# Optimization experiments

Measured on AMD Instinct MI355X. Metric: run time of the kernel, lower is better.

## Reference

```python
import jax, jax.numpy as jnp
import numpy as np

OBS_LEN, BATCH, IN_DIM, HID = 20, 2048, 512, 1024


def setup_inputs() -> dict:
    key = jax.random.key(0)
    ks = jax.random.split(key, 9)
    s_ih = 1.0 / np.sqrt(HID)  # torch LSTMCell init scale (uniform); use normal*scale for simplicity
    return {
        "obs_traj": jax.random.normal(ks[0], (OBS_LEN, BATCH, 2), jnp.float32),
        "h0": jax.random.normal(ks[1], (BATCH, HID), jnp.float32),
        "c0": jax.random.normal(ks[2], (BATCH, HID), jnp.float32),
        "W_emb": jax.random.normal(ks[3], (IN_DIM, 2), jnp.float32) * 0.5,
        "b_emb": jax.random.normal(ks[4], (IN_DIM,), jnp.float32) * 0.5,
        "W_ih": jax.random.normal(ks[5], (4 * HID, IN_DIM), jnp.float32) * s_ih,
        "W_hh": jax.random.normal(ks[6], (4 * HID, HID), jnp.float32) * s_ih,
        "b_ih": jax.random.normal(ks[7], (4 * HID,), jnp.float32) * s_ih,
        "b_hh": jax.random.normal(ks[8], (4 * HID,), jnp.float32) * s_ih,
    }


def reference(obs_traj, h0, c0, W_emb, b_emb, W_ih, W_hh, b_ih, b_hh):
    # input embedding: Linear(2 -> IN_DIM) applied to all timesteps at once
    # [T, B, 2] @ [2, IN_DIM] -> [T, B, IN_DIM]
    x_emb = jnp.einsum('tbi,hi->tbh', obs_traj, W_emb) + b_emb
    x_emb = x_emb[:OBS_LEN]

    H = h0.shape[-1]
    bias = b_ih + b_hh  # fold both biases once

    def step(carry, x_t):
        h, c = carry
        # gates: [B, 4H], PyTorch gate order i, f, g, o
        gates = x_t @ W_ih.T + h @ W_hh.T + bias
        i_g = jax.nn.sigmoid(gates[:, 0 * H:1 * H])
        f_g = jax.nn.sigmoid(gates[:, 1 * H:2 * H])
        g_g = jnp.tanh(gates[:, 2 * H:3 * H])
        o_g = jax.nn.sigmoid(gates[:, 3 * H:4 * H])
        c_new = f_g * c + i_g * g_g
        h_new = o_g * jnp.tanh(c_new)
        return (h_new, c_new), None

    (h_final, _), _ = jax.lax.scan(step, (h0, c0), x_emb)
    return h_final
```

## Files before the change

### kernel.cpp

```cpp
#include <hip/hip_runtime.h>

#define B_SZ 2048
#define HID  1024
#define G4   4096
#define IN_D 512
#define T_LEN 20

#define POFF(r, q) ((r)*32 + ((((q) ^ (((r) >> 1) & 3))) << 3))

typedef __attribute__((ext_vector_type(8))) _Float16 f16x8;
typedef __attribute__((ext_vector_type(4))) float f32x4;
typedef const __attribute__((address_space(1))) void* gas_p;
typedef __attribute__((address_space(3))) void* las_p;

__device__ __forceinline__ float bf2f(ushort u){
  union { unsigned int i; float f; } v; v.i = ((unsigned int)u) << 16; return v.f;
}
__device__ __forceinline__ ushort f2bf(float f){
  union { float f; unsigned int i; } v; v.f = f;
  unsigned int r = v.i + 0x7fffu + ((v.i >> 16) & 1u);
  return (ushort)(r >> 16);
}
__device__ __forceinline__ ushort f2h(float f){
  _Float16 h = (_Float16)f;
  union { _Float16 h; ushort u; } v; v.h = h; return v.u;
}
__device__ __forceinline__ float rdv(const void* p, long idx, int fl){
  return fl ? ((const float*)p)[idx] : bf2f(((const ushort*)p)[idx]);
}
__device__ __forceinline__ float sigm(float x){ return 1.0f/(1.0f + __expf(-x)); }
__device__ __forceinline__ float tanh_f(float x){
  float e = __expf(2.0f*x);
  return 1.0f - 2.0f/(e + 1.0f);
}

__global__ void detect_dtype(const ushort* __restrict__ h0bits, int* __restrict__ flag){
  int weird = 0;
  for (int i = 0; i < 256; i += 2){
    float a = fabsf(bf2f(h0bits[i]));
    if (!(a >= 1e-8f && a <= 1e4f)) weird++;
  }
  *flag = (weird >= 32) ? 1 : 0;
}

__global__ void canon(const void* __restrict__ h0, const void* __restrict__ c0,
                      const void* __restrict__ whh, const int* __restrict__ flag,
                      ushort* __restrict__ hA,
                      float* __restrict__ c_state,
                      ushort* __restrict__ wpk){
  const int fl = *flag;
  long i = (long)blockIdx.x * 256 + threadIdx.x;
  const long N1 = (long)B_SZ * HID;
  const long N3 = (long)G4 * HID;
  if (i < N1){
    const int b = (int)(i >> 10), j = (int)(i & 1023);
    const int r = b & 127, q = (j >> 3) & 3;
    const long po = ((long)(b >> 7)*32 + (j >> 5))*4096 + POFF(r, q) + (j & 7);
    hA[po] = f2h(rdv(h0, i, fl));
    return;
  }
  i -= N1;
  if (i < N1){ c_state[i] = rdv(c0, i, fl); return; }
  i -= N1;
  if (i < N3){
    const int n = (int)(i >> 10), k = (int)(i & 1023);
    const int g = n >> 10, j = n & 1023;
    const int nb = j >> 5, r = g*32 + (j & 31);
    const int kt = k >> 5, q = (k >> 3) & 3;
    const long base = ((long)(nb*32 + kt))*4096 + POFF(r, q) + (k & 7);
    wpk[base] = f2h(rdv(whh, i, fl));
  }
}

__global__ void fold_emb(const void* __restrict__ Wih, const void* __restrict__ Wemb,
                         const void* __restrict__ bemb, const void* __restrict__ bih,
                         const void* __restrict__ bhh, const int* __restrict__ flag,
                         float* __restrict__ M0, float* __restrict__ M1, float* __restrict__ Beff){
  const int n = blockIdx.x;
  const int lane = threadIdx.x;
  const int fl = *flag;
  float s0 = 0.f, s1 = 0.f, sb = 0.f;
  for (int j = lane; j < IN_D; j += 64){
    float w  = rdv(Wih, (long)n*IN_D + j, fl);
    float e0 = rdv(Wemb, 2L*j, fl);
    float e1 = rdv(Wemb, 2L*j + 1, fl);
    float be = rdv(bemb, j, fl);
    s0 += w*e0; s1 += w*e1; sb += w*be;
  }
  #pragma unroll
  for (int off = 32; off > 0; off >>= 1){
    s0 += __shfl_down(s0, off, 64);
    s1 += __shfl_down(s1, off, 64);
    sb += __shfl_down(sb, off, 64);
  }
  if (lane == 0){
    M0[n] = s0; M1[n] = s1;
    Beff[n] = sb + rdv(bih, n, fl) + rdv(bhh, n, fl);
  }
}

__global__ __launch_bounds__(256, 4)
void lstm_step(const ushort* __restrict__ hin, ushort* __restrict__ hout,
               void* __restrict__ out_final,
               float* __restrict__ c_state,
               const ushort* __restrict__ wpk,
               const float* __restrict__ M0, const float* __restrict__ M1,
               const float* __restrict__ Beff,
               const void* __restrict__ obs_raw, int t_step,
               const int* __restrict__ flag, int is_final)
{
  __shared__ __align__(16) ushort lds[2*8192];

  const int tid  = threadIdx.x;
  const int wave = tid >> 6;
  const int lane = tid & 63;
  const int l15  = lane & 15;
  const int quad = lane >> 4;
  const int wm   = wave & 1;
  const int wn   = wave >> 1;

  const int bid = blockIdx.x;
  const int xcd = bid & 7, u = bid >> 3;
  const int mb  = ((xcd & 1) << 3) | (u & 7);
  const int nb  = ((xcd >> 1) << 3) | (u >> 3);
  const int n0  = nb << 5;

  f32x4 acc[4][4];
  #pragma unroll
  for (int g = 0; g < 4; g++)
    #pragma unroll
    for (int mt = 0; mt < 4; mt++)
      acc[g][mt] = (f32x4){0.f, 0.f, 0.f, 0.f};

  const ushort* aB = hin + (size_t)mb*32*4096;
  const ushort* wB = wpk + (size_t)nb*32*4096;

  const int dOff = tid*8;

  #define DMA_TILE(kt, buf) do {                                              \
    const ushort* s0 = aB + (size_t)(kt)*4096;                                \
    const ushort* s1 = wB + (size_t)(kt)*4096;                                \
    ushort* d = &lds[(buf)*8192];                                             \
    __builtin_amdgcn_global_load_lds((gas_p)(s0+dOff),      (las_p)(d+dOff),      16,0,0); \
    __builtin_amdgcn_global_load_lds((gas_p)(s0+2048+dOff), (las_p)(d+2048+dOff), 16,0,0); \
    __builtin_amdgcn_global_load_lds((gas_p)(s1+dOff),      (las_p)(d+4096+dOff), 16,0,0); \
    __builtin_amdgcn_global_load_lds((gas_p)(s1+2048+dOff), (las_p)(d+6144+dOff), 16,0,0); \
  } while (0)

  int offA[4], offB[4];
  #pragma unroll
  for (int mt = 0; mt < 4; mt++) {
    const int r = wm*64 + mt*16 + l15;
    offA[mt] = POFF(r, quad);
  }
  #pragma unroll
  for (int g = 0; g < 4; g++) {
    const int r = g*32 + wn*16 + l15;
    offB[g] = 4096 + POFF(r, quad);
  }

  DMA_TILE(0, 0);

  #pragma unroll 1
  for (int kt = 0; kt < HID/32; kt++) {
    const int sb = (kt & 1) * 8192;
    __syncthreads();
    if (kt + 1 < HID/32) DMA_TILE(kt + 1, (kt + 1) & 1);

    f16x8 a[4], b[4];
    #pragma unroll
    for (int mt = 0; mt < 4; mt++)
      a[mt] = *reinterpret_cast<const f16x8*>(&lds[sb + offA[mt]]);
    #pragma unroll
    for (int g = 0; g < 4; g++)
      b[g] = *reinterpret_cast<const f16x8*>(&lds[sb + offB[g]]);

    #pragma unroll
    for (int g = 0; g < 4; g++)
      #pragma unroll
      for (int mt = 0; mt < 4; mt++)
        acc[g][mt] = __builtin_amdgcn_mfma_f32_16x16x32_f16(a[mt], b[g], acc[g][mt], 0, 0, 0);
  }

  const int fl = *flag;
  const int j = n0 + wn*16 + l15;
  float bi[4], m0v[4], m1v[4];
  #pragma unroll
  for (int g = 0; g < 4; g++) {
    bi[g]  = Beff[g*HID + j];
    m0v[g] = M0[g*HID + j];
    m1v[g] = M1[g*HID + j];
  }
  const int jq = (j >> 3) & 3;
  #pragma unroll
  for (int mt = 0; mt < 4; mt++) {
    #pragma unroll
    for (int r = 0; r < 4; r++) {
      const int bl7 = wm*64 + mt*16 + quad*4 + r;
      const int b   = mb*128 + bl7;
      const long oidx = ((long)t_step * B_SZ + b) * 2;
      const float o0 = rdv(obs_raw, oidx, fl);
      const float o1 = rdv(obs_raw, oidx + 1, fl);
      const size_t off = (size_t)b*HID + j;
      float pi = acc[0][mt][r] + o0*m0v[0] + o1*m1v[0] + bi[0];
      float pf = acc[1][mt][r] + o0*m0v[1] + o1*m1v[1] + bi[1];
      float pg = acc[2][mt][r] + o0*m0v[2] + o1*m1v[2] + bi[2];
      float po = acc[3][mt][r] + o0*m0v[3] + o1*m1v[3] + bi[3];
      float cn = sigm(pf)*c_state[off] + sigm(pi)*tanh_f(pg);
      float hn = sigm(po)*tanh_f(cn);
      c_state[off] = cn;
      if (is_final) {
        if (fl) ((float*)out_final)[off] = hn;
        else    ((ushort*)out_final)[off] = f2bf(hn);
      } else {
        const long hpo = ((long)mb*32 + (j >> 5))*4096 + POFF(bl7, jq) + (j & 7);
        hout[hpo] = f2h(hn);
      }
    }
  }
}

extern "C" void kernel_launch(void* const* d_in, const int* in_sizes, int n_in,
                              void* d_out, int out_size, void* d_ws, size_t ws_size,
                              hipStream_t stream) {
  const void* obs  = d_in[0];
  const void* h0   = d_in[1];
  const void* c0   = d_in[2];
  const void* Wemb = d_in[3];
  const void* bemb = d_in[4];
  const void* Wih  = d_in[5];
  const void* Whh  = d_in[6];
  const void* bih  = d_in[7];
  const void* bhh  = d_in[8];

  char* w = (char*)d_ws;
  int*    flag    = (int*)w;
  float*  M0      = (float*)(w + 256);
  float*  M1      = M0 + G4;
  float*  Beff    = M1 + G4;
  float*  c_state = Beff + G4;
  ushort* wpk     = (ushort*)(c_state + (size_t)B_SZ*HID);
  ushort* hA      = wpk + (size_t)G4*HID;
  ushort* hB      = hA + (size_t)B_SZ*HID;

  detect_dtype<<<1, 1, 0, stream>>>((const ushort*)h0, flag);

  long totalCanon = 2L*B_SZ*HID + (long)G4*HID;
  canon<<<(int)((totalCanon + 255)/256), 256, 0, stream>>>(
      h0, c0, Whh, flag, hA, c_state, wpk);

  fold_emb<<<G4, 64, 0, stream>>>(Wih, Wemb, bemb, bih, bhh, flag, M0, M1, Beff);

  for (int t = 0; t < T_LEN; t++) {
    const ushort* ih = (t & 1) ? hB : hA;
    ushort* oh = (t & 1) ? hA : hB;
    lstm_step<<<512, 256, 0, stream>>>(ih, oh, d_out, c_state,
                                       wpk, M0, M1, Beff,
                                       obs, t, flag, (t == T_LEN - 1) ? 1 : 0);
  }
}
```

Before: 654.4 us.

## Load A operand directly from global into registers, stage only weights in LDS

The hidden-state (A) tile is now read straight from global memory into registers with a one-step register double buffer, and only the weight (B) tile goes through LDS via async global-to-LDS loads. This halves LDS usage and LDS traffic per k-step, and it relaxes the occupancy hint in launch_bounds from 4 to 2. The risk is that direct global loads expose more latency than the LDS path. Each wave in the same wm row also now fetches its A fragments redundantly from global or cache.

```diff
diff --git a/kernel.cpp b/kernel.cpp
--- a/kernel.cpp
+++ b/kernel.cpp
@@ -99,7 +99,7 @@
   }
 }
 
-__global__ __launch_bounds__(256, 4)
+__global__ __launch_bounds__(256, 2)
 void lstm_step(const ushort* __restrict__ hin, ushort* __restrict__ hout,
                void* __restrict__ out_final,
                float* __restrict__ c_state,
@@ -109,7 +109,7 @@
                const void* __restrict__ obs_raw, int t_step,
                const int* __restrict__ flag, int is_final)
 {
-  __shared__ __align__(16) ushort lds[2*8192];
+  __shared__ __align__(16) ushort lds[2*4096];
 
   const int tid  = threadIdx.x;
   const int wave = tid >> 6;
@@ -137,14 +137,11 @@
 
   const int dOff = tid*8;
 
-  #define DMA_TILE(kt, buf) do {                                              \
-    const ushort* s0 = aB + (size_t)(kt)*4096;                                \
+  #define DMA_B(kt, buf) do {                                                 \
     const ushort* s1 = wB + (size_t)(kt)*4096;                                \
-    ushort* d = &lds[(buf)*8192];                                             \
-    __builtin_amdgcn_global_load_lds((gas_p)(s0+dOff),      (las_p)(d+dOff),      16,0,0); \
-    __builtin_amdgcn_global_load_lds((gas_p)(s0+2048+dOff), (las_p)(d+2048+dOff), 16,0,0); \
-    __builtin_amdgcn_global_load_lds((gas_p)(s1+dOff),      (las_p)(d+4096+dOff), 16,0,0); \
-    __builtin_amdgcn_global_load_lds((gas_p)(s1+2048+dOff), (las_p)(d+6144+dOff), 16,0,0); \
+    ushort* d = &lds[(buf)*4096];                                             \
+    __builtin_amdgcn_global_load_lds((gas_p)(s1+dOff),      (las_p)(d+dOff),      16,0,0); \
+    __builtin_amdgcn_global_load_lds((gas_p)(s1+2048+dOff), (las_p)(d+2048+dOff), 16,0,0); \
   } while (0)
 
   int offA[4], offB[4];
@@ -156,31 +153,44 @@
   #pragma unroll
   for (int g = 0; g < 4; g++) {
     const int r = g*32 + wn*16 + l15;
-    offB[g] = 4096 + POFF(r, quad);
-  }
-
-  DMA_TILE(0, 0);
+    offB[g] = POFF(r, quad);
+  }
+
+  f16x8 a0[4], a1[4];
+  #pragma unroll
+  for (int mt = 0; mt < 4; mt++)
+    a0[mt] = *reinterpret_cast<const f16x8*>(aB + offA[mt]);
+  DMA_B(0, 0);
+
+  #define KSTEP(kt, CUR, NXT) do {                                            \
+    __syncthreads();           \
+    if ((kt) + 1 < HID/32) {                                                  \
+      DMA_B((kt)+1, ((kt)+1) & 1);                                            \
+      const ushort* an = aB + (size_t)((kt)+1)*4096;                          \
+      NXT[0] = *reinterpret_cast<const f16x8*>(an + offA[0]);                 \
+      NXT[1] = *reinterpret_cast<const f16x8*>(an + offA[1]);                 \
+      NXT[2] = *reinterpret_cast<const f16x8*>(an + offA[2]);                 \
+      NXT[3] = *reinterpret_cast<const f16x8*>(an + offA[3]);                 \
+    }                                                                         \
+    const int sb_ = ((kt) & 1) * 4096;                                        \
+    f16x8 b[4];                                                               \
+    _Pragma("unroll")                                                         \
+    for (int g = 0; g < 4; g++)                                               \
+      b[g] = *reinterpret_cast<const f16x8*>(&lds[sb_ + offB[g]]);            \
+    _Pragma("unroll")                                                         \
+    for (int g = 0; g < 4; g++)                                               \
+      _Pragma("unroll")                                                       \
+      for (int mt = 0; mt < 4; mt++)                                          \
+        acc[g][mt] = __builtin_amdgcn_mfma_f32_16x16x32_f16(CUR[mt], b[g], acc[g][mt], 0, 0, 0); \
+  } while (0)
 
   #pragma unroll 1
-  for (int kt = 0; kt < HID/32; kt++) {
-    const int sb = (kt & 1) * 8192;
-    __syncthreads();
-    if (kt + 1 < HID/32) DMA_TILE(kt + 1, (kt + 1) & 1);
-
-    f16x8 a[4], b[4];
-    #pragma unroll
-    for (int mt = 0; mt < 4; mt++)
-      a[mt] = *reinterpret_cast<const f16x8*>(&lds[sb + offA[mt]]);
-    #pragma unroll
-    for (int g = 0; g < 4; g++)
-      b[g] = *reinterpret_cast<const f16x8*>(&lds[sb + offB[g]]);
-
-    #pragma unroll
-    for (int g = 0; g < 4; g++)
-      #pragma unroll
-      for (int mt = 0; mt < 4; mt++)
-        acc[g][mt] = __builtin_amdgcn_mfma_f32_16x16x32_f16(a[mt], b[g], acc[g][mt], 0, 0, 0);
-  }
+  for (int kt2 = 0; kt2 < HID/64; kt2++) {
+    KSTEP(2*kt2,     a0, a1);
+    KSTEP(2*kt2 + 1, a1, a0);
+  }
+  #undef KSTEP
+  #undef DMA_B
 
   const int fl = *flag;
   const int j = n0 + wn*16 + l15;
```

New measurement: 735.1 us. 1.12x slower.
